# Optimization experiments

Measured on AMD Instinct MI355X. Metric: run time of the kernel, lower is better.

## Reference

```python
import jax, jax.numpy as jnp
import numpy as np

B, T, D = 64, 8192, 128
UNITS = 128

def setup_inputs() -> dict:
    key = jax.random.key(0)
    k1, k2, k3 = jax.random.split(key, 3)
    inputs = jax.random.normal(k1, (B, T, D), dtype=jnp.float32)
    # Dense(units): kernel [D, units], bias [units]
    W_kernel = jax.random.normal(k2, (D, UNITS), dtype=jnp.float32) * (1.0 / np.sqrt(D))
    W_bias = jnp.zeros((UNITS,), dtype=jnp.float32)
    # Dense(1): kernel [units, 1], bias [1]
    V_kernel = jax.random.normal(k3, (UNITS, 1), dtype=jnp.float32) * (1.0 / np.sqrt(UNITS))
    V_bias = jnp.zeros((1,), dtype=jnp.float32)
    return {"inputs": inputs, "W_kernel": W_kernel, "W_bias": W_bias,
            "V_kernel": V_kernel, "V_bias": V_bias}

def reference(inputs, W_kernel, W_bias, V_kernel, V_bias):
    # score: [B, T, units]
    score = jnp.tanh(jnp.einsum('btd,du->btu', inputs, W_kernel) + W_bias)
    # logits: [B, T, 1]; softmax over time axis (axis=1)
    logits = jnp.einsum('btu,uo->bto', score, V_kernel) + V_bias
    attention_weights = jax.nn.softmax(logits, axis=1)
    # weighted sum over time -> [B, D]
    context_vector = jnp.sum(attention_weights * inputs, axis=1)
    return context_vector
```

## Files before the change

kernel.cpp:

```cpp
#include <hip/hip_runtime.h>
#include <hip/hip_bf16.h>

typedef __attribute__((ext_vector_type(8))) short short8;
typedef __attribute__((ext_vector_type(4))) float f32x4;
typedef __attribute__((ext_vector_type(4))) int int4v;

#define B_SZ 64
#define T_SZ 8192
#define D_SZ 128
#define U_SZ 128
#define T_TILE 64
#define GRID_P 512
#define TILES_PER_BLK 16
#define BLKS_PER_B 8
#define P_STRIDE 132
#define WT_LD 136
#define TANH_SCALE 2.8853900817779268f
#define DEFER_THR 8.0f

__device__ __forceinline__ unsigned short f2bf(float f) {
  unsigned int u = __builtin_bit_cast(unsigned int, f);
  u += 0x7fffu + ((u >> 16) & 1u);
  return (unsigned short)(u >> 16);
}

__device__ __forceinline__ float bf2f(unsigned short s) {
  return __builtin_bit_cast(float, (unsigned int)s << 16);
}

__device__ __forceinline__ float exp2_fast(float xs) {
  float e;
  asm("v_exp_f32 %0, %1" : "=v"(e) : "v"(xs));
  return e;
}

template<int CTRL>
__device__ __forceinline__ float dpp_add(float v) {
  int t = __builtin_amdgcn_update_dpp(0, __builtin_bit_cast(int, v),
                                      CTRL, 0xf, 0xf, true);
  return v + __builtin_bit_cast(float, t);
}
__device__ __forceinline__ float row_reduce16(float v) {
  v = dpp_add<0x118>(v);
  v = dpp_add<0x114>(v);
  v = dpp_add<0x112>(v);
  v = dpp_add<0x111>(v);
  return v;
}

__device__ __forceinline__ void cvt_tile(const f32x4 pf[8], short8 afrag[4]) {
#pragma unroll
  for (int kt = 0; kt < 4; ++kt) {
    f32x4 f0 = pf[kt * 2], f1 = pf[kt * 2 + 1];
    int w0, w1, w2, w3;
    asm("v_cvt_pk_bf16_f32 %0, %1, %2" : "=v"(w0) : "v"(f0[0]), "v"(f0[1]));
    asm("v_cvt_pk_bf16_f32 %0, %1, %2" : "=v"(w1) : "v"(f0[2]), "v"(f0[3]));
    asm("v_cvt_pk_bf16_f32 %0, %1, %2" : "=v"(w2) : "v"(f1[0]), "v"(f1[1]));
    asm("v_cvt_pk_bf16_f32 %0, %1, %2" : "=v"(w3) : "v"(f1[2]), "v"(f1[3]));
    int4v w = {w0, w1, w2, w3};
    afrag[kt] = __builtin_bit_cast(short8, w);
  }
}

__global__ void k_prep(const float* __restrict__ wk, unsigned short* __restrict__ wt) {
  int i = blockIdx.x * 256 + threadIdx.x;
  if (i < D_SZ * U_SZ) {
    int d = i >> 7, u = i & 127;
    wt[u * D_SZ + d] = f2bf(wk[i] * TANH_SCALE);
  }
}

__global__ __launch_bounds__(256) void k_partial(
    const float* __restrict__ x, const unsigned short* __restrict__ wt_g,
    const float* __restrict__ wb, const float* __restrict__ v,
    const float* __restrict__ vb, float* __restrict__ pbuf)
{
  __shared__ unsigned short wt[U_SZ][WT_LD];
  __shared__ float wb_s[U_SZ], v_s[U_SZ];
  __shared__ float logits[4][16];
  __shared__ float fin[4][D_SZ];
  __shared__ float fm[4], fs[4];

  const int tid  = threadIdx.x;
  const int bidx = blockIdx.x;

  for (int i = tid; i < U_SZ * 16; i += 256) {
    int row = i >> 4, c16 = i & 15;
    uint4 val = ((const uint4*)wt_g)[i];
    *(uint4*)&wt[row][c16 * 8] = val;
  }
  if (tid < U_SZ) { wb_s[tid] = wb[tid] * TANH_SCALE; v_s[tid] = v[tid]; }
  __syncthreads();

  const int w  = tid >> 6;
  const int l  = tid & 63;
  const int lr = l & 15;
  const int lh = l >> 4;
  const float vbias = vb[0];

  float vsum = 0.0f;
#pragma unroll
  for (int ut = 0; ut < 8; ++ut) vsum += v_s[ut * 16 + lr];

  const int b        = bidx >> 3;
  const int row0     = (bidx & (BLKS_PER_B - 1)) * (TILES_PER_BLK * T_TILE);
  const float* xbase = x + ((size_t)b * T_SZ + row0 + w * 16 + lr) * D_SZ + lh * 8;

  f32x4 pf[8];
#pragma unroll
  for (int kt = 0; kt < 4; ++kt) {
    pf[kt * 2]     = *(const f32x4*)(xbase + kt * 32);
    pf[kt * 2 + 1] = *(const f32x4*)(xbase + kt * 32 + 4);
  }
  short8 afrag[4];
  cvt_tile(pf, afrag);

  float m_run = -3.0e38f, s_run = 0.0f;
  float rc[4][8];
#pragma unroll
  for (int kt = 0; kt < 4; ++kt)
#pragma unroll
    for (int j = 0; j < 8; ++j) rc[kt][j] = 0.0f;

  for (int it = 0; it < TILES_PER_BLK; ++it) {
    if (it + 1 < TILES_PER_BLK) {
      const float* p = xbase + (size_t)(it + 1) * T_TILE * D_SZ;
#pragma unroll
      for (int kt = 0; kt < 4; ++kt) {
        pf[kt * 2]     = *(const f32x4*)(p + kt * 32);
        pf[kt * 2 + 1] = *(const f32x4*)(p + kt * 32 + 4);
      }
      __builtin_amdgcn_sched_barrier(0);
    }

    float lg[4] = {0.f, 0.f, 0.f, 0.f};
#pragma unroll
    for (int ut = 0; ut < 8; ++ut) {
      const float wbv = wb_s[ut * 16 + lr];
      f32x4 acc = {wbv, wbv, wbv, wbv};
#pragma unroll
      for (int kt = 0; kt < 4; ++kt) {
        short8 bfrag = *(const short8*)&wt[ut * 16 + lr][kt * 32 + lh * 8];
        acc = __builtin_amdgcn_mfma_f32_16x16x32_bf16(afrag[kt], bfrag, acc, 0, 0, 0);
      }
      const float vv = v_s[ut * 16 + lr];
#pragma unroll
      for (int r = 0; r < 4; ++r)
        lg[r] = fmaf(vv, __builtin_amdgcn_rcpf(exp2_fast(acc[r]) + 1.0f), lg[r]);
    }
#pragma unroll
    for (int r = 0; r < 4; ++r) {
      lg[r] = row_reduce16(fmaf(-2.0f, lg[r], vsum));
    }
    if (lr == 15) {
#pragma unroll
      for (int r = 0; r < 4; ++r)
        logits[w][lh * 4 + r] = lg[r] + vbias;
    }

    float lv = logits[w][lr];
    float mx = lv;
#pragma unroll
    for (int k = 1; k <= 8; k <<= 1) mx = fmaxf(mx, __shfl_xor(mx, k, 64));
    if (mx > m_run + DEFER_THR) {
      const float e_old = __expf(m_run - mx);
      s_run *= e_old;
#pragma unroll
      for (int kt = 0; kt < 4; ++kt)
#pragma unroll
        for (int j = 0; j < 8; ++j) rc[kt][j] *= e_old;
      m_run = mx;
    }
    const float pr = __expf(lv - m_run);
    float ss = pr;
#pragma unroll
    for (int k = 1; k <= 8; k <<= 1) ss += __shfl_xor(ss, k, 64);
    s_run += ss;

#pragma unroll
    for (int kt = 0; kt < 4; ++kt) {
#pragma unroll
      for (int j = 0; j < 8; ++j) {
        rc[kt][j] = fmaf(pr, bf2f((unsigned short)afrag[kt][j]), rc[kt][j]);
      }
    }

    __builtin_amdgcn_sched_barrier(0);
    if (it + 1 < TILES_PER_BLK) cvt_tile(pf, afrag);
  }

  if (l == 0) { fm[w] = m_run; fs[w] = s_run; }
  __syncthreads();
  const float m_blk = fmaxf(fmaxf(fm[0], fm[1]), fmaxf(fm[2], fm[3]));
  const float e_w   = __expf(m_run - m_blk);
#pragma unroll
  for (int kt = 0; kt < 4; ++kt) {
    float cs[8];
#pragma unroll
    for (int j = 0; j < 8; ++j) cs[j] = row_reduce16(rc[kt][j]);
    if (lr == 15) {
      f32x4 v0 = {cs[0] * e_w, cs[1] * e_w, cs[2] * e_w, cs[3] * e_w};
      f32x4 v1 = {cs[4] * e_w, cs[5] * e_w, cs[6] * e_w, cs[7] * e_w};
      *(f32x4*)&fin[w][kt * 32 + lh * 8]     = v0;
      *(f32x4*)&fin[w][kt * 32 + lh * 8 + 4] = v1;
    }
  }
  __syncthreads();

  float* pb = pbuf + (size_t)bidx * P_STRIDE;
  if (tid < 128) {
    pb[tid] = fin[0][tid] + fin[1][tid] + fin[2][tid] + fin[3][tid];
  } else if (tid == 128) {
    pb[128] = m_blk;
  } else if (tid == 129) {
    float sb = fs[0] * __expf(fm[0] - m_blk) + fs[1] * __expf(fm[1] - m_blk)
             + fs[2] * __expf(fm[2] - m_blk) + fs[3] * __expf(fm[3] - m_blk);
    pb[129] = sb;
  }
}

__global__ __launch_bounds__(128) void k_combine(const float* __restrict__ pbuf,
                                                 float* __restrict__ out)
{
  const int b = blockIdx.x, tid = threadIdx.x;
  __shared__ float sm[BLKS_PER_B], sden[BLKS_PER_B];
  const float* base = pbuf + (size_t)b * BLKS_PER_B * P_STRIDE;

  if (tid < BLKS_PER_B) {
    sm[tid]   = base[tid * P_STRIDE + 128];
    sden[tid] = base[tid * P_STRIDE + 129];
  }
  __syncthreads();

  float mx = -3.0e38f;
#pragma unroll
  for (int i = 0; i < BLKS_PER_B; ++i) mx = fmaxf(mx, sm[i]);
  float den = 0.0f, c = 0.0f;
#pragma unroll
  for (int i = 0; i < BLKS_PER_B; ++i) {
    float e = __expf(sm[i] - mx);
    den += sden[i] * e;
    c = fmaf(base[(size_t)i * P_STRIDE + tid], e, c);
  }
  out[b * D_SZ + tid] = c / den;
}

extern "C" void kernel_launch(void* const* d_in, const int* in_sizes, int n_in,
                              void* d_out, int out_size, void* d_ws, size_t ws_size,
                              hipStream_t stream) {
  const float* x  = (const float*)d_in[0];
  const float* wk = (const float*)d_in[1];
  const float* wb = (const float*)d_in[2];
  const float* vk = (const float*)d_in[3];
  const float* vb = (const float*)d_in[4];
  float* out = (float*)d_out;

  unsigned short* wt = (unsigned short*)d_ws;
  float* pbuf = (float*)((char*)d_ws + 32768);

  k_prep<<<64, 256, 0, stream>>>(wk, wt);
  k_partial<<<GRID_P, 256, 0, stream>>>(x, wt, wb, vk, vb, pbuf);
  k_combine<<<B_SZ, 128, 0, stream>>>(pbuf, out);
}
```

Baseline: 58.09 us.

## Fuse weight prep and combine into one kernel using atomic last-block ticket

Removes the separate weight-transpose kernel and the combine kernel. Each block now converts and transposes the fp32 W kernel into shared memory itself, and the last block per batch, picked by an atomic counter, does the cross-block softmax combine. A memset is added to clear the counters. This cuts two kernel launches and their dependency gaps, at the cost of redundant per-block weight conversion, strided shared-memory stores during the transpose, and threadfence/atomic overhead. The exp call is also switched from inline asm v_exp_f32 to exp2f.

```diff
diff --git a/kernel.cpp b/kernel.cpp
--- a/kernel.cpp
+++ b/kernel.cpp
@@ -1,5 +1,6 @@
 #include <hip/hip_runtime.h>
 #include <hip/hip_bf16.h>
+#include <cmath>
 
 typedef __attribute__((ext_vector_type(8))) short short8;
 typedef __attribute__((ext_vector_type(4))) float f32x4;
@@ -28,12 +29,6 @@
   return __builtin_bit_cast(float, (unsigned int)s << 16);
 }
 
-__device__ __forceinline__ float exp2_fast(float xs) {
-  float e;
-  asm("v_exp_f32 %0, %1" : "=v"(e) : "v"(xs));
-  return e;
-}
-
 template<int CTRL>
 __device__ __forceinline__ float dpp_add(float v) {
   int t = __builtin_amdgcn_update_dpp(0, __builtin_bit_cast(int, v),
@@ -62,32 +57,31 @@
   }
 }
 
-__global__ void k_prep(const float* __restrict__ wk, unsigned short* __restrict__ wt) {
-  int i = blockIdx.x * 256 + threadIdx.x;
-  if (i < D_SZ * U_SZ) {
-    int d = i >> 7, u = i & 127;
-    wt[u * D_SZ + d] = f2bf(wk[i] * TANH_SCALE);
-  }
-}
-
-__global__ __launch_bounds__(256) void k_partial(
-    const float* __restrict__ x, const unsigned short* __restrict__ wt_g,
+__global__ __launch_bounds__(256) void k_fused(
+    const float* __restrict__ x, const float* __restrict__ wk,
     const float* __restrict__ wb, const float* __restrict__ v,
-    const float* __restrict__ vb, float* __restrict__ pbuf)
+    const float* __restrict__ vb, float* __restrict__ pbuf,
+    int* __restrict__ cnt, float* __restrict__ out)
 {
   __shared__ unsigned short wt[U_SZ][WT_LD];
   __shared__ float wb_s[U_SZ], v_s[U_SZ];
   __shared__ float logits[4][16];
   __shared__ float fin[4][D_SZ];
   __shared__ float fm[4], fs[4];
+  __shared__ float sm2[BLKS_PER_B], sd2[BLKS_PER_B];
+  __shared__ int ticket;
 
   const int tid  = threadIdx.x;
   const int bidx = blockIdx.x;
 
-  for (int i = tid; i < U_SZ * 16; i += 256) {
-    int row = i >> 4, c16 = i & 15;
-    uint4 val = ((const uint4*)wt_g)[i];
-    *(uint4*)&wt[row][c16 * 8] = val;
+  for (int i = tid; i < (U_SZ * D_SZ) / 4; i += 256) {
+    const int d  = i >> 5;
+    const int u4 = (i & 31) * 4;
+    float4 f = *(const float4*)&wk[d * U_SZ + u4];
+    wt[u4 + 0][d] = f2bf(f.x * TANH_SCALE);
+    wt[u4 + 1][d] = f2bf(f.y * TANH_SCALE);
+    wt[u4 + 2][d] = f2bf(f.z * TANH_SCALE);
+    wt[u4 + 3][d] = f2bf(f.w * TANH_SCALE);
   }
   if (tid < U_SZ) { wb_s[tid] = wb[tid] * TANH_SCALE; v_s[tid] = v[tid]; }
   __syncthreads();
@@ -146,7 +140,7 @@
       const float vv = v_s[ut * 16 + lr];
 #pragma unroll
       for (int r = 0; r < 4; ++r)
-        lg[r] = fmaf(vv, __builtin_amdgcn_rcpf(exp2_fast(acc[r]) + 1.0f), lg[r]);
+        lg[r] = fmaf(vv, __builtin_amdgcn_rcpf(exp2f(acc[r]) + 1.0f), lg[r]);
     }
 #pragma unroll
     for (int r = 0; r < 4; ++r) {
@@ -217,32 +211,33 @@
              + fs[2] * __expf(fm[2] - m_blk) + fs[3] * __expf(fm[3] - m_blk);
     pb[129] = sb;
   }
-}
-
-__global__ __launch_bounds__(128) void k_combine(const float* __restrict__ pbuf,
-                                                 float* __restrict__ out)
-{
-  const int b = blockIdx.x, tid = threadIdx.x;
-  __shared__ float sm[BLKS_PER_B], sden[BLKS_PER_B];
-  const float* base = pbuf + (size_t)b * BLKS_PER_B * P_STRIDE;
-
-  if (tid < BLKS_PER_B) {
-    sm[tid]   = base[tid * P_STRIDE + 128];
-    sden[tid] = base[tid * P_STRIDE + 129];
-  }
-  __syncthreads();
-
-  float mx = -3.0e38f;
-#pragma unroll
-  for (int i = 0; i < BLKS_PER_B; ++i) mx = fmaxf(mx, sm[i]);
-  float den = 0.0f, c = 0.0f;
-#pragma unroll
-  for (int i = 0; i < BLKS_PER_B; ++i) {
-    float e = __expf(sm[i] - mx);
-    den += sden[i] * e;
-    c = fmaf(base[(size_t)i * P_STRIDE + tid], e, c);
-  }
-  out[b * D_SZ + tid] = c / den;
+
+  __threadfence();
+  __syncthreads();
+  if (tid == 0) ticket = atomicAdd(&cnt[b], 1);
+  __syncthreads();
+  if (ticket == BLKS_PER_B - 1) {
+    __threadfence();
+    const volatile float* base = pbuf + (size_t)b * BLKS_PER_B * P_STRIDE;
+    if (tid < BLKS_PER_B) {
+      sm2[tid] = base[tid * P_STRIDE + 128];
+      sd2[tid] = base[tid * P_STRIDE + 129];
+    }
+    __syncthreads();
+    if (tid < 128) {
+      float mx = sm2[0];
+#pragma unroll
+      for (int i = 1; i < BLKS_PER_B; ++i) mx = fmaxf(mx, sm2[i]);
+      float den = 0.0f, c = 0.0f;
+#pragma unroll
+      for (int i = 0; i < BLKS_PER_B; ++i) {
+        float e = __expf(sm2[i] - mx);
+        den += sd2[i] * e;
+        c = fmaf(base[(size_t)i * P_STRIDE + tid], e, c);
+      }
+      out[b * D_SZ + tid] = c / den;
+    }
+  }
 }
 
 extern "C" void kernel_launch(void* const* d_in, const int* in_sizes, int n_in,
@@ -255,10 +250,9 @@
   const float* vb = (const float*)d_in[4];
   float* out = (float*)d_out;
 
-  unsigned short* wt = (unsigned short*)d_ws;
-  float* pbuf = (float*)((char*)d_ws + 32768);
-
-  k_prep<<<64, 256, 0, stream>>>(wk, wt);
-  k_partial<<<GRID_P, 256, 0, stream>>>(x, wt, wb, vk, vb, pbuf);
-  k_combine<<<B_SZ, 128, 0, stream>>>(pbuf, out);
-}
+  int* cnt    = (int*)d_ws;
+  float* pbuf = (float*)((char*)d_ws + 512);
+
+  hipMemsetAsync(cnt, 0, B_SZ * sizeof(int), stream);
+  k_fused<<<GRID_P, 256, 0, stream>>>(x, wk, wb, vk, vb, pbuf, cnt, out);
+}
```

New measurement: 142.6 us. 2.45x slower.
